# Optimization experiments

Hardware: AMD Instinct MI355X
Metric: run time of the kernel (lower is better)

Reference implementation:

```python
import jax, jax.numpy as jnp
import numpy as np

T, S, B, D, H = 1024, 1024, 4, 512, 8
HD = D // H
DFF = 2048
W = 16  # sliding-window half-width -> band of 2W+1 keys per query
EPS = 1e-5
SCALE = 1.0 / float(np.sqrt(HD))


def setup_inputs():
    key = jax.random.key(0)
    ks = jax.random.split(key, 16)
    sc = 0.02
    def nrm(k, sh):
        return jax.random.normal(k, sh, jnp.float32) * sc
    z = lambda sh: jnp.zeros(sh, jnp.float32)
    o = lambda sh: jnp.ones(sh, jnp.float32)
    return {
        "tgt": nrm(ks[0], (T, B, D)),
        "memory": nrm(ks[1], (S, B, D)),
        "in_proj_w": nrm(ks[2], (3 * D, D)), "in_proj_b": z((3 * D,)),
        "out_proj_w": nrm(ks[3], (D, D)), "out_proj_b": z((D,)),
        "sw_q_w": nrm(ks[4], (D, D)), "sw_q_b": z((D,)),
        "sw_k_w": nrm(ks[5], (D, D)), "sw_k_b": z((D,)),
        "sw_v_w": nrm(ks[6], (D, D)), "sw_v_b": z((D,)),
        "sw_o_w": nrm(ks[7], (D, D)), "sw_o_b": z((D,)),
        "lin1_w": nrm(ks[8], (DFF, D)), "lin1_b": z((DFF,)),
        "lin2_w": nrm(ks[9], (D, DFF)), "lin2_b": z((D,)),
        "n1_g": o((D,)), "n1_b": z((D,)),
        "n2_g": o((D,)), "n2_b": z((D,)),
        "n3_g": o((D,)), "n3_b": z((D,)),
    }


def _ln(x, g, b):
    m = jnp.mean(x, -1, keepdims=True)
    v = jnp.mean(jnp.square(x - m), -1, keepdims=True)
    return (x - m) * jax.lax.rsqrt(v + EPS) * g + b


def _heads(x):  # [L,B,D] -> [L,B,H,HD]
    return x.reshape(x.shape[0], B, H, HD)


def _self_attn(x, wqkv, bqkv, wo, bo):
    # nn.MultiheadAttention, seq-first layout [T,B,D]
    qkv = jnp.einsum('tbd,ed->tbe', x, wqkv) + bqkv
    q, k, v = (_heads(a) for a in jnp.split(qkv, 3, axis=-1))
    scores = jnp.einsum('tbhd,sbhd->bhts', q, k) * SCALE
    attn = jax.nn.softmax(scores, -1)
    out = jnp.einsum('bhts,sbhd->tbhd', attn, v).reshape(T, B, D)
    return jnp.einsum('tbd,ed->tbe', out, wo) + bo


def _sliding_window_attn(x, mem, wq, bq, wk, bk, wv, bv, wo, bo):
    # banded cross-attention: query i attends to memory keys |i-j| <= W
    q = _heads(jnp.einsum('tbd,ed->tbe', x, wq) + bq)    # [T,B,H,HD]
    k = _heads(jnp.einsum('sbd,ed->sbe', mem, wk) + bk)  # [S,B,H,HD]
    v = _heads(jnp.einsum('sbd,ed->sbe', mem, wv) + bv)
    idx = jnp.arange(T)[:, None] + jnp.arange(-W, W + 1)[None, :]  # [T,2W+1]
    valid = (idx >= 0) & (idx < S)
    idxc = jnp.clip(idx, 0, S - 1)
    kb = k[idxc]  # [T,2W+1,B,H,HD] banded key gather (no dense TxS mask)
    vb = v[idxc]
    scores = jnp.einsum('tbhd,twbhd->bhtw', q, kb) * SCALE
    scores = jnp.where(valid[None, None, :, :], scores, -jnp.inf)
    attn = jax.nn.softmax(scores, -1)
    out = jnp.einsum('bhtw,twbhd->tbhd', attn, vb).reshape(T, B, D)
    return jnp.einsum('tbd,ed->tbe', out, wo) + bo


def reference(tgt, memory, in_proj_w, in_proj_b, out_proj_w, out_proj_b,
              sw_q_w, sw_q_b, sw_k_w, sw_k_b, sw_v_w, sw_v_b, sw_o_w, sw_o_b,
              lin1_w, lin1_b, lin2_w, lin2_b,
              n1_g, n1_b, n2_g, n2_b, n3_g, n3_b):
    # norm_first=False (post-norm) path, pattern='sliding_window', eval mode (dropout=0)
    x = tgt
    x = _ln(x + _self_attn(x, in_proj_w, in_proj_b, out_proj_w, out_proj_b), n1_g, n1_b)
    x = _ln(x + _sliding_window_attn(x, memory, sw_q_w, sw_q_b, sw_k_w, sw_k_b,
                                     sw_v_w, sw_v_b, sw_o_w, sw_o_b), n2_g, n2_b)
    h = jax.nn.relu(jnp.einsum('tbd,fd->tbf', x, lin1_w) + lin1_b)
    ff = jnp.einsum('tbf,df->tbd', h, lin2_w) + lin2_b
    x = _ln(x + ff, n3_g, n3_b)
    return x
```

## Files before the change

### kernel.cpp

```cpp
#include <hip/hip_runtime.h>

typedef unsigned short u16;
typedef unsigned int u32;

#define BATCH 4
#define NTOK 4096
#define SCALE_ATTN 0.125f

typedef float f32x4 __attribute__((ext_vector_type(4)));
typedef __bf16 bf16x8 __attribute__((ext_vector_type(8)));

__device__ __forceinline__ float b2f(u16 s) { return __uint_as_float(((u32)s) << 16); }
__device__ __forceinline__ u16 f2bf(float f) {
    u32 u = __float_as_uint(f);
    u += 0x7FFFu + ((u >> 16) & 1u);
    return (u16)(u >> 16);
}
__device__ __forceinline__ u32 pk2(float x, float y) {
    return (u32)f2bf(x) | ((u32)f2bf(y) << 16);
}
__device__ __forceinline__ u32 pk2t(float x, float y) {
    return (__float_as_uint(x) >> 16) | (__float_as_uint(y) & 0xFFFF0000u);
}
__device__ __forceinline__ uint4 pack8(float4 a, float4 b) {
    uint4 r;
    r.x = pk2(a.x, a.y); r.y = pk2(a.z, a.w);
    r.z = pk2(b.x, b.y); r.w = pk2(b.z, b.w);
    return r;
}
__device__ __forceinline__ f32x4 mfma16(uint4 a, uint4 b, f32x4 c) {
    return __builtin_amdgcn_mfma_f32_16x16x32_bf16(
        __builtin_bit_cast(bf16x8, a), __builtin_bit_cast(bf16x8, b), c, 0, 0, 0);
}

struct CvtTable {
    const float* src[10];
    u32 start[10];
};
__global__ __launch_bounds__(256) void cvt_bf16_kernel(CvtTable tab, u16* __restrict__ dst)
{
    u32 i8 = (blockIdx.x * 256u + threadIdx.x) * 8u;
    int t = 0;
    #pragma unroll
    for (int k = 1; k < 10; ++k) t += (i8 >= tab.start[k]) ? 1 : 0;
    const float* s = tab.src[t] + (i8 - tab.start[t]);
    float4 f0 = *(const float4*)s;
    float4 f1 = *(const float4*)(s + 4);
    *(uint4*)(dst + i8) = pack8(f0, f1);
}

template<int BM, int BN>
__global__ __launch_bounds__(256) void gemm_lds_kernel(
    const u16* __restrict__ A, const u16* __restrict__ B,
    const float* __restrict__ bias, u16* __restrict__ C,
    int M, int N, int K, int relu)
{
    constexpr int WMF = BM / 32;
    constexpr int WNF = BN / 32;
    constexpr int AIW = BM / 32;
    constexpr int BIW = BN / 32;

    __shared__ u16 As[BM * 64];
    __shared__ u16 Bs[BN * 64];

    const int tid = threadIdx.x;
    const int wave = tid >> 6, lane = tid & 63;
    const int lm = lane & 15, quad = lane >> 4;
    const int m0 = blockIdx.y * BM, n0 = blockIdx.x * BN;
    const int wr = wave >> 1, wc = wave & 1;
    const int lk = (lane >> 4) * 8;

    f32x4 acc[WMF][WNF] = {};

    for (int k0 = 0; k0 < K; k0 += 64) {
        #pragma unroll
        for (int t = 0; t < AIW; ++t) {
            int j = wave * AIW + t;
            int i = j >> 1, c = j & 1;
            const u16* gp = A + (size_t)(m0 + i * 16 + lm) * K + k0 + c * 32 + lk;
            __builtin_amdgcn_global_load_lds(
                (const __attribute__((address_space(1))) u32*)gp,
                (__attribute__((address_space(3))) u32*)(As + j * 512), 16, 0, 0);
        }
        #pragma unroll
        for (int t = 0; t < BIW; ++t) {
            int j = wave * BIW + t;
            int i = j >> 1, c = j & 1;
            const u16* gp = B + (size_t)(n0 + i * 16 + lm) * K + k0 + c * 32 + lk;
            __builtin_amdgcn_global_load_lds(
                (const __attribute__((address_space(1))) u32*)gp,
                (__attribute__((address_space(3))) u32*)(Bs + j * 512), 16, 0, 0);
        }
        __syncthreads();

        #pragma unroll
        for (int kk = 0; kk < 2; ++kk) {
            uint4 af[WMF], bf[WNF];
            #pragma unroll
            for (int i2 = 0; i2 < WMF; ++i2) {
                int g = wr * WMF + i2;
                af[i2] = *(const uint4*)(As + ((g * 8 + kk * 4 + quad) * 16 + lm) * 8);
            }
            #pragma unroll
            for (int j2 = 0; j2 < WNF; ++j2) {
                int g = wc * WNF + j2;
                bf[j2] = *(const uint4*)(Bs + ((g * 8 + kk * 4 + quad) * 16 + lm) * 8);
            }
            #pragma unroll
            for (int i2 = 0; i2 < WMF; ++i2)
                #pragma unroll
                for (int j2 = 0; j2 < WNF; ++j2)
                    acc[i2][j2] = mfma16(af[i2], bf[j2], acc[i2][j2]);
        }
        __syncthreads();
    }

    #pragma unroll
    for (int j2 = 0; j2 < WNF; ++j2) {
        int cg = n0 + (wc * WNF + j2) * 16 + lm;
        float bv = bias ? bias[cg] : 0.f;
        #pragma unroll
        for (int i2 = 0; i2 < WMF; ++i2) {
            #pragma unroll
            for (int r = 0; r < 4; ++r) {
                int rg = m0 + (wr * WMF + i2) * 16 + quad * 4 + r;
                float v = acc[i2][j2][r] + bv;
                if (relu) v = fmaxf(v, 0.f);
                C[(size_t)rg * N + cg] = f2bf(v);
            }
        }
    }
}

__global__ __launch_bounds__(256) void add_ln_kernel(
    const u16* __restrict__ a, const void* __restrict__ r,
    const float* __restrict__ g, const float* __restrict__ be,
    void* __restrict__ out, int r_f32, int out_f32)
{
    const int row = blockIdx.x, tid = threadIdx.x;
    u32 av = *(const u32*)(a + (size_t)row * 512 + tid * 2);
    float r0, r1;
    if (r_f32) {
        float2 rv = *(const float2*)((const float*)r + (size_t)row * 512 + tid * 2);
        r0 = rv.x; r1 = rv.y;
    } else {
        u32 rv = *(const u32*)((const u16*)r + (size_t)row * 512 + tid * 2);
        r0 = b2f((u16)(rv & 0xFFFFu)); r1 = b2f((u16)(rv >> 16));
    }
    float v0 = b2f((u16)(av & 0xFFFFu)) + r0;
    float v1 = b2f((u16)(av >> 16)) + r1;
    float s = v0 + v1, q = v0 * v0 + v1 * v1;
    #pragma unroll
    for (int m = 1; m < 64; m <<= 1) { s += __shfl_xor(s, m); q += __shfl_xor(q, m); }
    __shared__ float ss[4], qq[4];
    int wave = tid >> 6, lane = tid & 63;
    if (lane == 0) { ss[wave] = s; qq[wave] = q; }
    __syncthreads();
    s = ss[0] + ss[1] + ss[2] + ss[3];
    q = qq[0] + qq[1] + qq[2] + qq[3];
    float mean = s * (1.f / 512.f);
    float var = q * (1.f / 512.f) - mean * mean;
    float rstd = rsqrtf(var + 1e-5f);
    float2 gv = *(const float2*)(g + tid * 2);
    float2 bv = *(const float2*)(be + tid * 2);
    float o0 = (v0 - mean) * rstd * gv.x + bv.x;
    float o1 = (v1 - mean) * rstd * gv.y + bv.y;
    if (out_f32) {
        float2 ov; ov.x = o0; ov.y = o1;
        *(float2*)((float*)out + (size_t)row * 512 + tid * 2) = ov;
    } else {
        *(u32*)((u16*)out + (size_t)row * 512 + tid * 2) = pk2(o0, o1);
    }
}

__global__ __launch_bounds__(256) void self_attn_kernel(
    const u16* __restrict__ qkv, u16* __restrict__ o)
{
    const int qb = blockIdx.x;
    const int bh = blockIdx.y;
    const int b = bh >> 3, h = bh & 7;
    const int tid = threadIdx.x;
    const int lane = tid & 63, wave = tid >> 6;
    const int lm = lane & 15, quad = lane >> 4;

    __shared__ u16 Ks[64 * 64];
    __shared__ u16 Vt[64][72];

    const int qrow0 = qb * 64 + wave * 16;
    const u16* qp = qkv + ((size_t)(qrow0 + lm) * BATCH + b) * 1536 + h * 64;
    uint4 qf0 = *(const uint4*)(qp + quad * 8);
    uint4 qf1 = *(const uint4*)(qp + 32 + quad * 8);

    f32x4 o4[4] = {};
    float m_s = -1e30f, l_s = 0.f;

    for (int c0 = 0; c0 < 1024; c0 += 64) {
        #pragma unroll
        for (int t2 = 0; t2 < 2; ++t2) {
            int j = wave * 2 + t2;
            int g = j >> 1, c = j & 1;
            const u16* gp = qkv + ((size_t)(c0 + g * 16 + lm) * BATCH + b) * 1536
                            + 512 + h * 64 + c * 32 + quad * 8;
            __builtin_amdgcn_global_load_lds(
                (const __attribute__((address_space(1))) u32*)gp,
                (__attribute__((address_space(3))) u32*)(Ks + j * 512), 16, 0, 0);
        }
        #pragma unroll
        for (int i = 0; i < 2; ++i) {
            int c = tid + i * 256;
            int key = c & 63, dv = (c >> 6) * 8;
            uint4 u = *(const uint4*)(
                qkv + ((size_t)(c0 + key) * BATCH + b) * 1536 + 1024 + h * 64 + dv);
            Vt[dv + 0][key] = (u16)(u.x & 0xFFFFu);
            Vt[dv + 1][key] = (u16)(u.x >> 16);
            Vt[dv + 2][key] = (u16)(u.y & 0xFFFFu);
            Vt[dv + 3][key] = (u16)(u.y >> 16);
            Vt[dv + 4][key] = (u16)(u.z & 0xFFFFu);
            Vt[dv + 5][key] = (u16)(u.z >> 16);
            Vt[dv + 6][key] = (u16)(u.w & 0xFFFFu);
            Vt[dv + 7][key] = (u16)(u.w >> 16);
        }
        __syncthreads();

        f32x4 s[4] = {};
        #pragma unroll
        for (int t = 0; t < 4; ++t) {
            uint4 k0 = *(const uint4*)(Ks + t * 1024 + quad * 128 + lm * 8);
            uint4 k1 = *(const uint4*)(Ks + t * 1024 + 512 + quad * 128 + lm * 8);
            s[t] = mfma16(k0, qf0, s[t]);
            s[t] = mfma16(k1, qf1, s[t]);
        }

        float mx = -1e30f;
        #pragma unroll
        for (int t = 0; t < 4; ++t)
            #pragma unroll
            for (int r = 0; r < 4; ++r) {
                s[t][r] *= SCALE_ATTN;
                mx = fmaxf(mx, s[t][r]);
            }
        mx = fmaxf(mx, __shfl_xor(mx, 16));
        mx = fmaxf(mx, __shfl_xor(mx, 32));
        float mn = fmaxf(m_s, mx);
        float alpha = __expf(m_s - mn);
        m_s = mn;
        float ps = 0.f;
        u32 pkx[4], pky[4];
        #pragma unroll
        for (int t = 0; t < 4; ++t) {
            float p0 = __expf(s[t][0] - mn);
            float p1 = __expf(s[t][1] - mn);
            float p2 = __expf(s[t][2] - mn);
            float p3 = __expf(s[t][3] - mn);
            ps += (p0 + p1) + (p2 + p3);
            pkx[t] = pk2t(p0, p1);
            pky[t] = pk2t(p2, p3);
        }
        ps += __shfl_xor(ps, 16);
        ps += __shfl_xor(ps, 32);
        l_s = l_s * alpha + ps;
        float av[4];
        #pragma unroll
        for (int r = 0; r < 4; ++r) av[r] = __shfl(alpha, quad * 20 + r);
        #pragma unroll
        for (int t = 0; t < 4; ++t)
            #pragma unroll
            for (int r = 0; r < 4; ++r) o4[t][r] *= av[r];

        #pragma unroll
        for (int kh = 0; kh < 2; ++kh) {
            int src1 = lm + 32 * (quad & 1);
            int src2 = src1 + 16;
            u32 xA = (u32)__shfl((int)pkx[2 * kh], src1);
            u32 xB = (u32)__shfl((int)pkx[2 * kh + 1], src1);
            u32 yA = (u32)__shfl((int)pky[2 * kh], src1);
            u32 yB = (u32)__shfl((int)pky[2 * kh + 1], src1);
            u32 zA = (u32)__shfl((int)pkx[2 * kh], src2);
            u32 zB = (u32)__shfl((int)pkx[2 * kh + 1], src2);
            u32 wA = (u32)__shfl((int)pky[2 * kh], src2);
            u32 wB = (u32)__shfl((int)pky[2 * kh + 1], src2);
            bool hiq = quad >= 2;
            uint4 pf;
            pf.x = hiq ? xB : xA;
            pf.y = hiq ? yB : yA;
            pf.z = hiq ? zB : zA;
            pf.w = hiq ? wB : wA;
            #pragma unroll
            for (int t = 0; t < 4; ++t) {
                uint4 vf = *(const uint4*)(&Vt[t * 16 + lm][kh * 32 + quad * 8]);
                o4[t] = mfma16(pf, vf, o4[t]);
            }
        }
        __syncthreads();
    }

    float linv = 1.f / l_s;
    float lv[4];
    #pragma unroll
    for (int r = 0; r < 4; ++r) lv[r] = __shfl(linv, quad * 20 + r);
    #pragma unroll
    for (int t = 0; t < 4; ++t) {
        #pragma unroll
        for (int r = 0; r < 4; ++r) {
            int row = qrow0 + quad * 4 + r;
            o[((size_t)row * BATCH + b) * 512 + h * 64 + t * 16 + lm] =
                f2bf(o4[t][r] * lv[r]);
        }
    }
}

__global__ __launch_bounds__(256) void sw_attn_kernel(
    const u16* __restrict__ q2, const u16* __restrict__ k2,
    const u16* __restrict__ v2, u16* __restrict__ o)
{
    const int qb = blockIdx.x;
    const int bh = blockIdx.y;
    const int b = bh >> 3, h = bh & 7;
    const int tid = threadIdx.x;
    const int lane = tid & 63, wave = tid >> 6;
    const int lm = lane & 15, quad = lane >> 4;

    __shared__ u16 Ks[14 * 512];
    __shared__ u16 Vt[64][120];

    const int kbase = qb * 64 - 16;
    const int qrow0 = qb * 64 + wave * 16;

    const u16* qp = q2 + ((size_t)(qrow0 + lm) * BATCH + b) * 512 + h * 64;
    uint4 qf0 = *(const uint4*)(qp + quad * 8);
    uint4 qf1 = *(const uint4*)(qp + 32 + quad * 8);

    #pragma unroll
    for (int t2 = 0; t2 < 4; ++t2) {
        int j = wave * 4 + t2;
        if (j < 14) {
            int g = j >> 1, c = j & 1;
            int key = kbase + g * 16 + lm;
            key = min(max(key, 0), 1023);
            const u16* gp = k2 + ((size_t)key * BATCH + b) * 512 + h * 64
                            + c * 32 + quad * 8;
            __builtin_amdgcn_global_load_lds(
                (const __attribute__((address_space(1))) u32*)gp,
                (__attribute__((address_space(3))) u32*)(Ks + j * 512), 16, 0, 0);
        }
    }
    #pragma unroll
    for (int i = 0; i < 4; ++i) {
        int c = tid + i * 256;
        if (c < 896) {
            int key = c >> 3, dv = (c & 7) * 8;
            int j = kbase + key;
            j = min(max(j, 0), 1023);
            uint4 u = *(const uint4*)(v2 + ((size_t)j * BATCH + b) * 512 + h * 64 + dv);
            Vt[dv + 0][key] = (u16)(u.x & 0xFFFFu);
            Vt[dv + 1][key] = (u16)(u.x >> 16);
            Vt[dv + 2][key] = (u16)(u.y & 0xFFFFu);
            Vt[dv + 3][key] = (u16)(u.y >> 16);
            Vt[dv + 4][key] = (u16)(u.z & 0xFFFFu);
            Vt[dv + 5][key] = (u16)(u.z >> 16);
            Vt[dv + 6][key] = (u16)(u.w & 0xFFFFu);
            Vt[dv + 7][key] = (u16)(u.w >> 16);
        }
    }
    __syncthreads();

    f32x4 s[4] = {};
    #pragma unroll
    for (int t = 0; t < 4; ++t) {
        int tw = wave + t;
        uint4 k0 = *(const uint4*)(Ks + (tw * 2 + 0) * 512 + quad * 128 + lm * 8);
        uint4 k1 = *(const uint4*)(Ks + (tw * 2 + 1) * 512 + quad * 128 + lm * 8);
        s[t] = mfma16(k0, qf0, s[t]);
        s[t] = mfma16(k1, qf1, s[t]);
    }

    float mx = -1e30f;
    #pragma unroll
    for (int t = 0; t < 4; ++t) {
        #pragma unroll
        for (int r = 0; r < 4; ++r) {
            int kl = t * 16 + quad * 4 + r;
            int jj = qrow0 - 16 + kl;
            int d = kl - lm;
            bool valid = (d >= 0) && (d <= 32) && (jj >= 0) && (jj < 1024);
            s[t][r] = valid ? s[t][r] * SCALE_ATTN : -1e30f;
            mx = fmaxf(mx, s[t][r]);
        }
    }
    mx = fmaxf(mx, __shfl_xor(mx, 16));
    mx = fmaxf(mx, __shfl_xor(mx, 32));
    float ps = 0.f;
    u32 pkx[4], pky[4];
    #pragma unroll
    for (int t = 0; t < 4; ++t) {
        float p0 = __expf(s[t][0] - mx);
        float p1 = __expf(s[t][1] - mx);
        float p2 = __expf(s[t][2] - mx);
        float p3 = __expf(s[t][3] - mx);
        ps += (p0 + p1) + (p2 + p3);
        pkx[t] = pk2t(p0, p1);
        pky[t] = pk2t(p2, p3);
    }
    ps += __shfl_xor(ps, 16);
    ps += __shfl_xor(ps, 32);

    f32x4 o4[4] = {};
    #pragma unroll
    for (int kh = 0; kh < 2; ++kh) {
        int src1 = lm + 32 * (quad & 1);
        int src2 = src1 + 16;
        u32 xA = (u32)__shfl((int)pkx[2 * kh], src1);
        u32 xB = (u32)__shfl((int)pkx[2 * kh + 1], src1);
        u32 yA = (u32)__shfl((int)pky[2 * kh], src1);
        u32 yB = (u32)__shfl((int)pky[2 * kh + 1], src1);
        u32 zA = (u32)__shfl((int)pkx[2 * kh], src2);
        u32 zB = (u32)__shfl((int)pkx[2 * kh + 1], src2);
        u32 wA = (u32)__shfl((int)pky[2 * kh], src2);
        u32 wB = (u32)__shfl((int)pky[2 * kh + 1], src2);
        bool hiq = quad >= 2;
        uint4 pf;
        pf.x = hiq ? xB : xA;
        pf.y = hiq ? yB : yA;
        pf.z = hiq ? zB : zA;
        pf.w = hiq ? wB : wA;
        #pragma unroll
        for (int t = 0; t < 4; ++t) {
            uint4 vf = *(const uint4*)(&Vt[t * 16 + lm][wave * 16 + kh * 32 + quad * 8]);
            o4[t] = mfma16(pf, vf, o4[t]);
        }
    }

    float linv = 1.f / ps;
    float lv[4];
    #pragma unroll
    for (int r = 0; r < 4; ++r) lv[r] = __shfl(linv, quad * 20 + r);
    #pragma unroll
    for (int t = 0; t < 4; ++t) {
        #pragma unroll
        for (int r = 0; r < 4; ++r) {
            int row = qrow0 + quad * 4 + r;
            o[((size_t)row * BATCH + b) * 512 + h * 64 + t * 16 + lm] =
                f2bf(o4[t][r] * lv[r]);
        }
    }
}

static inline void gemm128(hipStream_t st, const u16* A, const u16* B, const float* bias,
                           u16* C, int M, int N, int K, int relu)
{
    dim3 g(N / 128, M / 128);
    gemm_lds_kernel<128, 128><<<g, dim3(256), 0, st>>>(A, B, bias, C, M, N, K, relu);
}
static inline void gemm64(hipStream_t st, const u16* A, const u16* B, const float* bias,
                          u16* C, int M, int N, int K, int relu)
{
    dim3 g(N / 64, M / 64);
    gemm_lds_kernel<64, 64><<<g, dim3(256), 0, st>>>(A, B, bias, C, M, N, K, relu);
}

extern "C" void kernel_launch(void* const* d_in, const int* in_sizes, int n_in,
                              void* d_out, int out_size, void* d_ws, size_t ws_size,
                              hipStream_t stream)
{
    const float* tgt        = (const float*)d_in[0];
    const float* memory     = (const float*)d_in[1];
    const float* in_proj_w  = (const float*)d_in[2];
    const float* in_proj_b  = (const float*)d_in[3];
    const float* out_proj_w = (const float*)d_in[4];
    const float* out_proj_b = (const float*)d_in[5];
    const float* sw_q_w = (const float*)d_in[6];
    const float* sw_q_b = (const float*)d_in[7];
    const float* sw_k_w = (const float*)d_in[8];
    const float* sw_k_b = (const float*)d_in[9];
    const float* sw_v_w = (const float*)d_in[10];
    const float* sw_v_b = (const float*)d_in[11];
    const float* sw_o_w = (const float*)d_in[12];
    const float* sw_o_b = (const float*)d_in[13];
    const float* lin1_w = (const float*)d_in[14];
    const float* lin1_b = (const float*)d_in[15];
    const float* lin2_w = (const float*)d_in[16];
    const float* lin2_b = (const float*)d_in[17];
    const float* n1_g = (const float*)d_in[18];
    const float* n1_b = (const float*)d_in[19];
    const float* n2_g = (const float*)d_in[20];
    const float* n2_b = (const float*)d_in[21];
    const float* n3_g = (const float*)d_in[22];
    const float* n3_b = (const float*)d_in[23];

    u16* ws = (u16*)d_ws;
    u16* qkv  = ws;
    u16* x1   = ws + 6291456;
    u16* bufA = ws + 8388608;
    u16* bufB = ws + 10485760;
    u16* x2   = ws + 12582912;
    u16* q2 = qkv;
    u16* k2 = qkv + 2097152;
    u16* v2 = qkv + 4194304;
    u16* hbuf = qkv;

    u16* wc = ws + 14680064;
    u16* tgtb  = wc;
    u16* memb  = wc + 2097152;
    u16* inpb  = wc + 4194304;
    u16* outpb = wc + 4980736;
    u16* swqb  = wc + 5242880;
    u16* swkb  = wc + 5505024;
    u16* swvb  = wc + 5767168;
    u16* swob  = wc + 6029312;
    u16* l1b   = wc + 6291456;
    u16* l2b   = wc + 7340032;

    CvtTable tab;
    const float* srcs[10] = {tgt, memory, in_proj_w, out_proj_w, sw_q_w,
                             sw_k_w, sw_v_w, sw_o_w, lin1_w, lin2_w};
    const u32 starts[10] = {0, 2097152, 4194304, 4980736, 5242880,
                            5505024, 5767168, 6029312, 6291456, 7340032};
    for (int i = 0; i < 10; ++i) { tab.src[i] = srcs[i]; tab.start[i] = starts[i]; }
    cvt_bf16_kernel<<<dim3(4096), dim3(256), 0, stream>>>(tab, wc);

    gemm128(stream, tgtb, inpb, in_proj_b, qkv, NTOK, 1536, 512, 0);
    self_attn_kernel<<<dim3(16, 32), dim3(256), 0, stream>>>(qkv, bufA);
    gemm64(stream, bufA, outpb, out_proj_b, bufB, NTOK, 512, 512, 0);
    add_ln_kernel<<<dim3(NTOK), dim3(256), 0, stream>>>(bufB, tgt, n1_g, n1_b, x1, 1, 0);
    gemm64(stream, x1, swqb, sw_q_b, q2, NTOK, 512, 512, 0);
    gemm64(stream, memb, swkb, sw_k_b, k2, NTOK, 512, 512, 0);
    gemm64(stream, memb, swvb, sw_v_b, v2, NTOK, 512, 512, 0);
    sw_attn_kernel<<<dim3(16, 32), dim3(256), 0, stream>>>(q2, k2, v2, bufA);
    gemm64(stream, bufA, swob, sw_o_b, bufB, NTOK, 512, 512, 0);
    add_ln_kernel<<<dim3(NTOK), dim3(256), 0, stream>>>(bufB, x1, n2_g, n2_b, x2, 0, 0);
    gemm128(stream, x2, l1b, lin1_b, hbuf, NTOK, 2048, 512, 1);
    gemm64(stream, hbuf, l2b, lin2_b, bufA, NTOK, 512, 2048, 0);
    add_ln_kernel<<<dim3(NTOK), dim3(256), 0, stream>>>(bufA, x2, n3_g, n3_b, d_out, 0, 1);
}
```

Measured before the change: 308.5 us.

## Double-buffer GEMM LDS tiles and fuse K/V projections into one GEMM

The GEMM kernel now uses two LDS buffers per operand and issues the next K-tile's global-to-LDS loads before computing on the current one. This drops the trailing barrier so memory latency can overlap MFMA work. The sliding-window K and V projections are merged into a single 1024-wide GEMM with a split bias, and the attention kernel reads from the interleaved KV buffer. The first residual layernorm now reads the bf16 copy of tgt instead of fp32. Costs are doubled LDS use, which may lower occupancy for 128x128 tiles, and slightly reduced residual precision.

```diff
diff --git a/kernel.cpp b/kernel.cpp
--- a/kernel.cpp
+++ b/kernel.cpp
@@ -52,16 +52,16 @@
 template<int BM, int BN>
 __global__ __launch_bounds__(256) void gemm_lds_kernel(
     const u16* __restrict__ A, const u16* __restrict__ B,
-    const float* __restrict__ bias, u16* __restrict__ C,
-    int M, int N, int K, int relu)
+    const float* __restrict__ bias, const float* __restrict__ bias2, int split,
+    u16* __restrict__ C, int M, int N, int K, int relu)
 {
     constexpr int WMF = BM / 32;
     constexpr int WNF = BN / 32;
     constexpr int AIW = BM / 32;
     constexpr int BIW = BN / 32;
 
-    __shared__ u16 As[BM * 64];
-    __shared__ u16 Bs[BN * 64];
+    __shared__ u16 As[2][BM * 64];
+    __shared__ u16 Bs[2][BN * 64];
 
     const int tid = threadIdx.x;
     const int wave = tid >> 6, lane = tid & 63;
@@ -72,7 +72,7 @@
 
     f32x4 acc[WMF][WNF] = {};
 
-    for (int k0 = 0; k0 < K; k0 += 64) {
+    auto stage = [&](int buf, int k0) {
         #pragma unroll
         for (int t = 0; t < AIW; ++t) {
             int j = wave * AIW + t;
@@ -80,7 +80,7 @@
             const u16* gp = A + (size_t)(m0 + i * 16 + lm) * K + k0 + c * 32 + lk;
             __builtin_amdgcn_global_load_lds(
                 (const __attribute__((address_space(1))) u32*)gp,
-                (__attribute__((address_space(3))) u32*)(As + j * 512), 16, 0, 0);
+                (__attribute__((address_space(3))) u32*)(&As[buf][j * 512]), 16, 0, 0);
         }
         #pragma unroll
         for (int t = 0; t < BIW; ++t) {
@@ -89,22 +89,27 @@
             const u16* gp = B + (size_t)(n0 + i * 16 + lm) * K + k0 + c * 32 + lk;
             __builtin_amdgcn_global_load_lds(
                 (const __attribute__((address_space(1))) u32*)gp,
-                (__attribute__((address_space(3))) u32*)(Bs + j * 512), 16, 0, 0);
-        }
+                (__attribute__((address_space(3))) u32*)(&Bs[buf][j * 512]), 16, 0, 0);
+        }
+    };
+
+    stage(0, 0);
+    int cur = 0;
+    for (int k0 = 0; k0 < K; k0 += 64) {
         __syncthreads();
-
+        if (k0 + 64 < K) stage(cur ^ 1, k0 + 64);
         #pragma unroll
         for (int kk = 0; kk < 2; ++kk) {
             uint4 af[WMF], bf[WNF];
             #pragma unroll
             for (int i2 = 0; i2 < WMF; ++i2) {
                 int g = wr * WMF + i2;
-                af[i2] = *(const uint4*)(As + ((g * 8 + kk * 4 + quad) * 16 + lm) * 8);
+                af[i2] = *(const uint4*)(&As[cur][((g * 8 + kk * 4 + quad) * 16 + lm) * 8]);
             }
             #pragma unroll
             for (int j2 = 0; j2 < WNF; ++j2) {
                 int g = wc * WNF + j2;
-                bf[j2] = *(const uint4*)(Bs + ((g * 8 + kk * 4 + quad) * 16 + lm) * 8);
+                bf[j2] = *(const uint4*)(&Bs[cur][((g * 8 + kk * 4 + quad) * 16 + lm) * 8]);
             }
             #pragma unroll
             for (int i2 = 0; i2 < WMF; ++i2)
@@ -112,13 +117,13 @@
                 for (int j2 = 0; j2 < WNF; ++j2)
                     acc[i2][j2] = mfma16(af[i2], bf[j2], acc[i2][j2]);
         }
-        __syncthreads();
+        cur ^= 1;
     }
 
     #pragma unroll
     for (int j2 = 0; j2 < WNF; ++j2) {
         int cg = n0 + (wc * WNF + j2) * 16 + lm;
-        float bv = bias ? bias[cg] : 0.f;
+        float bv = (cg < split) ? bias[cg] : bias2[cg - split];
         #pragma unroll
         for (int i2 = 0; i2 < WMF; ++i2) {
             #pragma unroll
@@ -310,8 +315,7 @@
 }
 
 __global__ __launch_bounds__(256) void sw_attn_kernel(
-    const u16* __restrict__ q2, const u16* __restrict__ k2,
-    const u16* __restrict__ v2, u16* __restrict__ o)
+    const u16* __restrict__ q2, const u16* __restrict__ kv, u16* __restrict__ o)
 {
     const int qb = blockIdx.x;
     const int bh = blockIdx.y;
@@ -337,7 +341,7 @@
             int g = j >> 1, c = j & 1;
             int key = kbase + g * 16 + lm;
             key = min(max(key, 0), 1023);
-            const u16* gp = k2 + ((size_t)key * BATCH + b) * 512 + h * 64
+            const u16* gp = kv + ((size_t)key * BATCH + b) * 1024 + h * 64
                             + c * 32 + quad * 8;
             __builtin_amdgcn_global_load_lds(
                 (const __attribute__((address_space(1))) u32*)gp,
@@ -351,7 +355,7 @@
             int key = c >> 3, dv = (c & 7) * 8;
             int j = kbase + key;
             j = min(max(j, 0), 1023);
-            uint4 u = *(const uint4*)(v2 + ((size_t)j * BATCH + b) * 512 + h * 64 + dv);
+            uint4 u = *(const uint4*)(kv + ((size_t)j * BATCH + b) * 1024 + 512 + h * 64 + dv);
             Vt[dv + 0][key] = (u16)(u.x & 0xFFFFu);
             Vt[dv + 1][key] = (u16)(u.x >> 16);
             Vt[dv + 2][key] = (u16)(u.y & 0xFFFFu);
@@ -445,17 +449,20 @@
     }
 }
 
-static inline void gemm128(hipStream_t st, const u16* A, const u16* B, const float* bias,
+static inline void gemm128(hipStream_t st, const u16* A, const u16* B,
+                           const float* bias, const float* bias2, int split,
                            u16* C, int M, int N, int K, int relu)
 {
     dim3 g(N / 128, M / 128);
-    gemm_lds_kernel<128, 128><<<g, dim3(256), 0, st>>>(A, B, bias, C, M, N, K, relu);
-}
-static inline void gemm64(hipStream_t st, const u16* A, const u16* B, const float* bias,
-                          u16* C, int M, int N, int K, int relu)
+    gemm_lds_kernel<128, 128><<<g, dim3(256), 0, st>>>(A, B, bias, bias2, split,
+                                                       C, M, N, K, relu);
+}
+static inline void gemm64(hipStream_t st, const u16* A, const u16* B,
+                          const float* bias, u16* C, int M, int N, int K, int relu)
 {
     dim3 g(N / 64, M / 64);
-    gemm_lds_kernel<64, 64><<<g, dim3(256), 0, st>>>(A, B, bias, C, M, N, K, relu);
+    gemm_lds_kernel<64, 64><<<g, dim3(256), 0, st>>>(A, B, bias, bias, N,
+                                                     C, M, N, K, relu);
 }
 
 extern "C" void kernel_launch(void* const* d_in, const int* in_sizes, int n_in,
@@ -494,8 +501,7 @@
     u16* bufB = ws + 10485760;
     u16* x2   = ws + 12582912;
     u16* q2 = qkv;
-    u16* k2 = qkv + 2097152;
-    u16* v2 = qkv + 4194304;
+    u16* kv = qkv + 2097152;
     u16* hbuf = qkv;
 
     u16* wc = ws + 14680064;
@@ -509,6 +515,7 @@
     u16* swob  = wc + 6029312;
     u16* l1b   = wc + 6291456;
     u16* l2b   = wc + 7340032;
+    (void)swvb;
 
     CvtTable tab;
     const float* srcs[10] = {tgt, memory, in_proj_w, out_proj_w, sw_q_w,
@@ -518,17 +525,16 @@
     for (int i = 0; i < 10; ++i) { tab.src[i] = srcs[i]; tab.start[i] = starts[i]; }
     cvt_bf16_kernel<<<dim3(4096), dim3(256), 0, stream>>>(tab, wc);
 
-    gemm128(stream, tgtb, inpb, in_proj_b, qkv, NTOK, 1536, 512, 0);
+    gemm128(stream, tgtb, inpb, in_proj_b, in_proj_b, 1536, qkv, NTOK, 1536, 512, 0);
     self_attn_kernel<<<dim3(16, 32), dim3(256), 0, stream>>>(qkv, bufA);
     gemm64(stream, bufA, outpb, out_proj_b, bufB, NTOK, 512, 512, 0);
-    add_ln_kernel<<<dim3(NTOK), dim3(256), 0, stream>>>(bufB, tgt, n1_g, n1_b, x1, 1, 0);
+    add_ln_kernel<<<dim3(NTOK), dim3(256), 0, stream>>>(bufB, tgtb, n1_g, n1_b, x1, 0, 0);
     gemm64(stream, x1, swqb, sw_q_b, q2, NTOK, 512, 512, 0);
-    gemm64(stream, memb, swkb, sw_k_b, k2, NTOK, 512, 512, 0);
-    gemm64(stream, memb, swvb, sw_v_b, v2, NTOK, 512, 512, 0);
-    sw_attn_kernel<<<dim3(16, 32), dim3(256), 0, stream>>>(q2, k2, v2, bufA);
+    gemm128(stream, memb, swkb, sw_k_b, sw_v_b, 512, kv, NTOK, 1024, 512, 0);
+    sw_attn_kernel<<<dim3(16, 32), dim3(256), 0, stream>>>(q2, kv, bufA);
     gemm64(stream, bufA, swob, sw_o_b, bufB, NTOK, 512, 512, 0);
     add_ln_kernel<<<dim3(NTOK), dim3(256), 0, stream>>>(bufB, x1, n2_g, n2_b, x2, 0, 0);
-    gemm128(stream, x2, l1b, lin1_b, hbuf, NTOK, 2048, 512, 1);
+    gemm128(stream, x2, l1b, lin1_b, lin1_b, 2048, hbuf, NTOK, 2048, 512, 1);
     gemm64(stream, hbuf, l2b, lin2_b, bufA, NTOK, 512, 2048, 0);
     add_ln_kernel<<<dim3(NTOK), dim3(256), 0, stream>>>(bufA, x2, n3_g, n3_b, d_out, 0, 1);
 }
```

Result: no change. 307.3 us (-0.4%).
